# Optimization experiments

Hardware: AMD Instinct MI355X
Metric: run time of the kernel (lower is better)

The kernel has to match this reference:

```python
import jax, jax.numpy as jnp
import numpy as np

BN_EPS = 1e-5


def setup_inputs() -> dict:
    key = jax.random.key(0)
    ks = jax.random.split(key, 8)
    B, C, H, W = 8, 512, 48, 48
    P = 64
    s_in = 1.0 / np.sqrt(C)
    s_p = 1.0 / np.sqrt(P)
    return {
        "x": jax.random.normal(ks[0], (B, C, H, W), dtype=jnp.float32),
        "Wq": jax.random.uniform(ks[1], (P, C), jnp.float32, -s_in, s_in),
        "Wk": jax.random.uniform(ks[2], (P, C), jnp.float32, -s_in, s_in),
        "Wv": jax.random.uniform(ks[3], (C, C), jnp.float32, -s_in, s_in),
        "align_w": jax.random.uniform(ks[4], (P,), jnp.float32, -s_p, s_p),
        "Wfc": jax.random.uniform(ks[5], (C, C), jnp.float32, -s_in, s_in),
        "bfc": jax.random.uniform(ks[6], (C,), jnp.float32, -s_in, s_in),
        "gamma": jnp.ones((C,), jnp.float32),
        "beta": jnp.zeros((C,), jnp.float32),
    }


def reference(x, Wq, Wk, Wv, align_w, Wfc, bfc, gamma, beta):
    B, C, H, W = x.shape
    N = H * W
    px = jnp.transpose(x.reshape(B, C, N), (0, 2, 1))  # [B, N, C]

    q = jnp.tanh(px @ Wq.T)  # [B, N, P]
    k = jnp.tanh(px @ Wk.T)  # [B, N, P]
    v = px @ Wv.T            # [B, N, C]

    # align(q_i * k_j) = sum_p q[b,i,p] * k[b,j,p] * align_w[p]
    scores = jnp.einsum('bip,bjp,p->bij', q, k, align_w)  # [B, N, N]
    attn = jax.nn.softmax(scores, axis=2)

    content = px + attn @ v           # [B, N, C]
    content = content @ Wfc.T + bfc   # fc
    c = jnp.transpose(content, (0, 2, 1)).reshape(B, C, H, W)

    # BatchNorm2d in training mode: batch statistics over (B, H, W), biased var
    mean = jnp.mean(c, axis=(0, 2, 3), keepdims=True)
    var = jnp.var(c, axis=(0, 2, 3), keepdims=True)
    g = gamma.reshape(1, C, 1, 1)
    b = beta.reshape(1, C, 1, 1)
    out = g * (c - mean) * jax.lax.rsqrt(var + BN_EPS) + b
    return jax.nn.relu(out)
```

## Files before the change

kernel.cpp:

```cpp
#include <hip/hip_runtime.h>
#include <stdint.h>

#define BB 8
#define CC 512
#define NN 2304
#define NT16 (NN / 16)
#define NT32 (NN / 32)
#define CT32 (CC / 32)
#define NYB 48

typedef float f32x4 __attribute__((ext_vector_type(4)));
typedef short s16x8 __attribute__((ext_vector_type(8)));

__device__ __forceinline__ unsigned short f2bf(float f) {
  union { float f; uint32_t u; } v; v.f = f;
  uint32_t u = v.u;
  return (unsigned short)((u + 0x7FFFu + ((u >> 16) & 1u)) >> 16);
}
__device__ __forceinline__ float bf2f(unsigned short b) {
  union { uint32_t u; float f; } v; v.u = ((uint32_t)b) << 16;
  return v.f;
}
__device__ __forceinline__ uint32_t cvtpk(float lo, float hi) {
  uint32_t r;
  asm("v_cvt_pk_bf16_f32 %0, %1, %2" : "=v"(r) : "v"(lo), "v"(hi));
  return r;
}


__global__ void k_prep_w(const float* __restrict__ Wq, const float* __restrict__ Wk,
                         const float* __restrict__ Wv, const float* __restrict__ Wfc,
                         unsigned short* __restrict__ wcat_t, unsigned short* __restrict__ wfc_t) {
  int idx = blockIdx.x * 256 + threadIdx.x;
  const int tot_cat = 640 * 512;
  if (idx < tot_cat) {
    int tile = idx >> 9, inner = idx & 511;
    int j = (tile >> 4) * 16 + (inner >> 5);
    int k = (tile & 15) * 32 + (inner & 31);
    float v = (j < 64) ? Wq[j * 512 + k] : ((j < 128) ? Wk[(j - 64) * 512 + k] : Wv[(j - 128) * 512 + k]);
    wcat_t[idx] = f2bf(v);
  } else if (idx < tot_cat + 512 * 512) {
    int i2 = idx - tot_cat;
    int tile = i2 >> 9, inner = i2 & 511;
    int j = (tile >> 4) * 16 + (inner >> 5);
    int k = (tile & 15) * 32 + (inner & 31);
    wfc_t[i2] = f2bf(Wfc[j * 512 + k]);
  }
}

__global__ void k_px(const float* __restrict__ x, unsigned short* __restrict__ px_t) {
  __shared__ float t[32][33];
  int b = blockIdx.x;
  int nb = blockIdx.y * 32;
  int cb = blockIdx.z * 32;
  int lane = threadIdx.x & 31;
  int row = threadIdx.x >> 5;
  const float* xb = x + (size_t)b * CC * NN;
  for (int rr = 0; rr < 4; rr++) {
    int c = cb + row + 8 * rr;
    t[row + 8 * rr][lane] = xb[(size_t)c * NN + nb + lane];
  }
  __syncthreads();
  int rbase = (b * NN + nb) >> 4;
  int ct = cb >> 5;
  for (int rr = 0; rr < 4; rr++) {
    int nl = row + 8 * rr;
    size_t off = ((size_t)(rbase + (nl >> 4)) * CT32 + ct) * 512 + (nl & 15) * 32 + lane;
    px_t[off] = f2bf(t[lane][nl]);
  }
}

__global__ __launch_bounds__(256, 2) void k_qkv(const unsigned short* __restrict__ px_t,
                                                const unsigned short* __restrict__ wcat_t,
                                                const float* __restrict__ align_w,
                                                unsigned short* __restrict__ q_t,
                                                unsigned short* __restrict__ k_t,
                                                unsigned short* __restrict__ vt_t) {
  int bid = blockIdx.x;
  int b = bid & 7;
  int t = bid >> 3;
  int z = t % 3;
  int nb = (t / 3) * 64;
  int tid = threadIdx.x;
  int w = tid >> 6, l = tid & 63, l15 = l & 15, lq = l >> 4;
  int loff = l15 * 32 + 8 * lq;
  int rA = (b * NN + nb) >> 4;
  int nfmax = (z == 0) ? 2 : 4;
  int rowB0 = (z == 0) ? 2 * w : 8 + (z - 1) * 16 + 4 * w;
  f32x4 acc[4][4];
  for (int mf = 0; mf < 4; mf++) for (int nf = 0; nf < 4; nf++) acc[mf][nf] = (f32x4){0.f, 0.f, 0.f, 0.f};
  for (int kk = 0; kk < 16; kk++) {
    s16x8 a[4], bbf[4];
    for (int mf = 0; mf < 4; mf++)
      a[mf] = *(const s16x8*)(px_t + ((size_t)(rA + mf) * CT32 + kk) * 512 + loff);
    for (int nf = 0; nf < 4; nf++)
      if (nf < nfmax)
        bbf[nf] = *(const s16x8*)(wcat_t + ((size_t)(rowB0 + nf) * CT32 + kk) * 512 + loff);
    for (int mf = 0; mf < 4; mf++)
      for (int nf = 0; nf < 4; nf++)
        if (nf < nfmax)
          acc[mf][nf] = __builtin_amdgcn_mfma_f32_16x16x32_bf16(a[mf], bbf[nf], acc[mf][nf], 0, 0, 0);
  }
  if (z == 0) {
    for (int mf = 0; mf < 4; mf++)
      for (int nf = 0; nf < 2; nf++)
        for (int r = 0; r < 4; r++) {
          int j = 32 * w + 16 * nf + l15;
          int nl = 4 * lq + r;
          float v = tanhf(acc[mf][nf][r]);
          if (w < 2) {
            v *= align_w[j];
            q_t[((size_t)(rA + mf) * 2 + w) * 512 + nl * 32 + (j & 31)] = f2bf(v);
          } else {
            k_t[((size_t)(rA + mf) * 2 + (w - 2)) * 512 + nl * 32 + (j & 31)] = f2bf(v);
          }
        }
  } else {
    unsigned short* vtb = vt_t + (size_t)b * (CC / 16) * NT32 * 512;
    for (int mf = 0; mf < 4; mf++)
      for (int nf = 0; nf < 4; nf++) {
        int c = (z - 1) * 256 + 64 * w + 16 * nf + l15;
        uint2 pp;
        pp.x = cvtpk(acc[mf][nf][0], acc[mf][nf][1]);
        pp.y = cvtpk(acc[mf][nf][2], acc[mf][nf][3]);
        int nlo = 16 * (mf & 1) + 4 * lq;
        size_t off = ((size_t)(c >> 4) * NT32 + (nb >> 5) + (mf >> 1)) * 512 + (c & 15) * 32 + nlo;
        *(uint2*)(vtb + off) = pp;
      }
  }
}

__global__ __launch_bounds__(256, 3) void k_attn(const unsigned short* __restrict__ q_t,
                                                 const unsigned short* __restrict__ k_t,
                                                 const unsigned short* __restrict__ vt_t,
                                                 unsigned short* __restrict__ px_t ) {
  __shared__ __align__(16) unsigned short e_s[2][48 * 64];
  __shared__ float rs_s[4][48];
  int bid = blockIdx.x;
  int b = bid & 7;
  int ch = ((bid >> 3) & 1) * 256;
  int ib = (bid >> 4) * 48;
  int tid = threadIdx.x;
  int w = tid >> 6, l = tid & 63, l15 = l & 15, lq = l >> 4;
  int c0 = ch + 64 * w;
  int loff = l15 * 32 + 8 * lq;
  int rQ = (b * NN + ib) >> 4;
  int ktb = b * NT16;
  const unsigned short* vb = vt_t + (size_t)b * (CC / 16) * NT32 * 512;

  s16x8 qa[3][2];
  for (int mf = 0; mf < 3; mf++)
    for (int ks = 0; ks < 2; ks++)
      qa[mf][ks] = *(const s16x8*)(q_t + ((size_t)(rQ + mf) * 2 + ks) * 512 + loff);

  f32x4 acc[3][4];
  for (int mf = 0; mf < 3; mf++) for (int nf = 0; nf < 4; nf++) acc[mf][nf] = (f32x4){0.f, 0.f, 0.f, 0.f};
  float rs[3] = {0.f, 0.f, 0.f};

  s16x8 kf0[2], kf1[2];
  for (int ks = 0; ks < 2; ks++)
    kf0[ks] = *(const s16x8*)(k_t + ((size_t)(ktb + w) * 2 + ks) * 512 + loff);

  auto step = [&](int jt, char* ebuf, s16x8 (&kfu)[2], s16x8 (&kfl)[2]) {
    int jtn = (jt < NN / 64 - 1) ? jt + 1 : jt;
    s16x8 vf[2][4];
    for (int ks = 0; ks < 2; ks++)
      for (int nf = 0; nf < 4; nf++)
        vf[ks][nf] = *(const s16x8*)(vb + ((size_t)((c0 >> 4) + nf) * NT32 + jt * 2 + ks) * 512 + loff);
    for (int ks = 0; ks < 2; ks++)
      kfl[ks] = *(const s16x8*)(k_t + ((size_t)(ktb + jtn * 4 + w) * 2 + ks) * 512 + loff);
    f32x4 sc[3];
    for (int mf = 0; mf < 3; mf++) sc[mf] = (f32x4){0.f, 0.f, 0.f, 0.f};
    __builtin_amdgcn_s_setprio(1);
    for (int ks = 0; ks < 2; ks++)
      for (int mf = 0; mf < 3; mf++)
        sc[mf] = __builtin_amdgcn_mfma_f32_16x16x32_bf16(kfu[ks], qa[mf][ks], sc[mf], 0, 0, 0);
    __builtin_amdgcn_s_setprio(0);
    for (int mf = 0; mf < 3; mf++) {
      float e0 = __expf(sc[mf][0]), e1 = __expf(sc[mf][1]);
      float e2 = __expf(sc[mf][2]), e3 = __expf(sc[mf][3]);
      rs[mf] += (e0 + e1) + (e2 + e3);
      uint2 pp;
      pp.x = cvtpk(e0, e1);
      pp.y = cvtpk(e2, e3);
      int i_ = 16 * mf + l15;
      int byte = (i_ * 128 + (16 * w + 4 * lq) * 2) ^ ((i_ & 7) << 4);
      *(uint2*)(ebuf + byte) = pp;
    }
    asm volatile("s_waitcnt lgkmcnt(0)" ::: "memory");
    __builtin_amdgcn_s_barrier();
    __builtin_amdgcn_sched_barrier(0);
    for (int ks = 0; ks < 2; ks++) {
      s16x8 ef[3];
      for (int mf = 0; mf < 3; mf++) {
        int i_ = 16 * mf + l15;
        int byte = (i_ * 128 + 64 * ks + 16 * lq) ^ ((i_ & 7) << 4);
        ef[mf] = *(const s16x8*)((const char*)ebuf + byte);
      }
      __builtin_amdgcn_s_setprio(1);
      for (int nf = 0; nf < 4; nf++)
        for (int mf = 0; mf < 3; mf++)
          acc[mf][nf] = __builtin_amdgcn_mfma_f32_16x16x32_bf16(ef[mf], vf[ks][nf], acc[mf][nf], 0, 0, 0);
      __builtin_amdgcn_s_setprio(0);
    }
  };

  for (int jt = 0; jt < NN / 64; jt += 2) {
    step(jt, (char*)e_s[0], kf0, kf1);
    step(jt + 1, (char*)e_s[1], kf1, kf0);
  }

  for (int mf = 0; mf < 3; mf++) {
    float v = rs[mf];
    v += __shfl_xor(v, 16);
    v += __shfl_xor(v, 32);
    rs[mf] = v;
  }
  if (lq == 0)
    for (int mf = 0; mf < 3; mf++)
      rs_s[w][16 * mf + l15] = rs[mf];
  __syncthreads();
  float inv[3][4];
  for (int mf = 0; mf < 3; mf++)
    for (int r = 0; r < 4; r++) {
      int i = 16 * mf + 4 * lq + r;
      inv[mf][r] = 1.0f / (rs_s[0][i] + rs_s[1][i] + rs_s[2][i] + rs_s[3][i]);
    }
  for (int mf = 0; mf < 3; mf++)
    for (int nf = 0; nf < 4; nf++)
      for (int r = 0; r < 4; r++) {
        int i = 16 * mf + 4 * lq + r;
        int bn = b * NN + ib + i;
        int c = c0 + 16 * nf + l15;
        size_t off = ((size_t)(bn >> 4) * CT32 + (c >> 5)) * 512 + (bn & 15) * 32 + (c & 31);
        px_t[off] = f2bf(bf2f(px_t[off]) + acc[mf][nf][r] * inv[mf][r]);
      }
}

__global__ __launch_bounds__(256, 3) void k_fc(const unsigned short* __restrict__ px_t,
                                               const unsigned short* __restrict__ wfc_t,
                                               const float* __restrict__ bfc,
                                               unsigned short* __restrict__ c16,
                                               float2* __restrict__ partials) {
  __shared__ float pss[4][32], psq[4][32];
  int bid = blockIdx.x;
  int s_ = bid >> 3;
  int yb = (bid & 7) + 8 * (s_ % 6);
  int cb = (s_ / 6) * 32;
  int fb = yb * 384;
  int tid = threadIdx.x;
  int w = tid >> 6, l = tid & 63, l15 = l & 15, lq = l >> 4;
  int fw = fb + 96 * w;
  int loff = l15 * 32 + 8 * lq;
  f32x4 acc[2][6];
  for (int mf = 0; mf < 2; mf++) for (int nf = 0; nf < 6; nf++) acc[mf][nf] = (f32x4){0.f, 0.f, 0.f, 0.f};
  for (int kk = 0; kk < 16; kk++) {
    s16x8 a[2], bbf[6];
    for (int mf = 0; mf < 2; mf++)
      a[mf] = *(const s16x8*)(wfc_t + ((size_t)((cb >> 4) + mf) * CT32 + kk) * 512 + loff);
    for (int nf = 0; nf < 6; nf++)
      bbf[nf] = *(const s16x8*)(px_t + ((size_t)((fw >> 4) + nf) * CT32 + kk) * 512 + loff);
    for (int mf = 0; mf < 2; mf++)
      for (int nf = 0; nf < 6; nf++)
        acc[mf][nf] = __builtin_amdgcn_mfma_f32_16x16x32_bf16(a[mf], bbf[nf], acc[mf][nf], 0, 0, 0);
  }
  float s8[2][4], q8[2][4];
  for (int mf = 0; mf < 2; mf++)
    for (int r = 0; r < 4; r++) {
      int c2 = cb + 16 * mf + 4 * lq + r;
      float bias = bfc[c2];
      float s = 0.f, q = 0.f;
      for (int nf = 0; nf < 6; nf++) {
        float v = acc[mf][nf][r] + bias;
        int flat = fw + 16 * nf + l15;
        int b2 = flat / NN;
        int n = flat - b2 * NN;
        c16[((size_t)b2 * CC + c2) * NN + n] = f2bf(v);
        s += v; q += v * v;
      }
      s8[mf][r] = s; q8[mf][r] = q;
    }
  for (int mf = 0; mf < 2; mf++)
    for (int r = 0; r < 4; r++) {
      float s = s8[mf][r], q = q8[mf][r];
      s += __shfl_xor(s, 1); q += __shfl_xor(q, 1);
      s += __shfl_xor(s, 2); q += __shfl_xor(q, 2);
      s += __shfl_xor(s, 4); q += __shfl_xor(q, 4);
      s += __shfl_xor(s, 8); q += __shfl_xor(q, 8);
      s8[mf][r] = s; q8[mf][r] = q;
    }
  if (l15 == 0)
    for (int mf = 0; mf < 2; mf++)
      for (int r = 0; r < 4; r++) {
        int idx = 16 * mf + 4 * lq + r;
        pss[w][idx] = s8[mf][r];
        psq[w][idx] = q8[mf][r];
      }
  __syncthreads();
  if (tid < 32) {
    float s = pss[0][tid] + pss[1][tid] + pss[2][tid] + pss[3][tid];
    float q = psq[0][tid] + psq[1][tid] + psq[2][tid] + psq[3][tid];
    partials[(size_t)(cb + tid) * NYB + yb] = make_float2(s, q);
  }
}

__global__ void k_stats2(const float2* __restrict__ partials, const float* __restrict__ gamma,
                         const float* __restrict__ beta, float2* __restrict__ ab) {
  int c = blockIdx.x * 256 + threadIdx.x;
  if (c >= CC) return;
  float s = 0.f, q = 0.f;
  for (int i = 0; i < NYB; i++) {
    float2 p = partials[(size_t)c * NYB + i];
    s += p.x; q += p.y;
  }
  const float invn = 1.0f / (BB * NN);
  float mean = s * invn;
  float var = q * invn - mean * mean;
  float a = gamma[c] * rsqrtf(var + 1e-5f);
  ab[c] = make_float2(a, beta[c] - mean * a);
}

__global__ void k_bn(const unsigned short* __restrict__ c16, float* __restrict__ out,
                     const float2* __restrict__ ab) {
  int idx = blockIdx.x * 256 + threadIdx.x;
  const int total = BB * CC * NN / 8;
  if (idx >= total) return;
  int c = (idx / (NN / 8)) & (CC - 1);
  float2 p = ab[c];
  s16x8 v = ((const s16x8*)c16)[idx];
  f32x4 o0, o1;
  for (int i = 0; i < 4; i++) o0[i] = fmaxf(0.f, bf2f((unsigned short)v[i]) * p.x + p.y);
  for (int i = 0; i < 4; i++) o1[i] = fmaxf(0.f, bf2f((unsigned short)v[4 + i]) * p.x + p.y);
  ((f32x4*)out)[idx * 2] = o0;
  ((f32x4*)out)[idx * 2 + 1] = o1;
}

extern "C" void kernel_launch(void* const* d_in, const int* in_sizes, int n_in,
                              void* d_out, int out_size, void* d_ws, size_t ws_size,
                              hipStream_t stream) {
  const float* x = (const float*)d_in[0];
  const float* Wq = (const float*)d_in[1];
  const float* Wk = (const float*)d_in[2];
  const float* Wv = (const float*)d_in[3];
  const float* align_w = (const float*)d_in[4];
  const float* Wfc = (const float*)d_in[5];
  const float* bfc = (const float*)d_in[6];
  const float* gamma = (const float*)d_in[7];
  const float* beta = (const float*)d_in[8];
  float* out = (float*)d_out;

  char* ws = (char*)d_ws;
  const size_t sz_px = (size_t)BB * NN * CC * 2;
  const size_t sz_q = (size_t)BB * NN * 64 * 2;
  const size_t sz_vr = (size_t)BB * NN * CC * 2;
  unsigned short* px_t = (unsigned short*)(ws);
  unsigned short* q_t = (unsigned short*)(ws + sz_px);
  unsigned short* k_t = (unsigned short*)(ws + sz_px + sz_q);
  unsigned short* c16 = (unsigned short*)(ws + sz_px + 2 * sz_q);
  unsigned short* vt_t = (unsigned short*)(ws + sz_px + 2 * sz_q + sz_vr);
  unsigned short* wcat_t = (unsigned short*)(ws + sz_px + 2 * sz_q + 2 * sz_vr);
  unsigned short* wfc_t = (unsigned short*)(ws + sz_px + 2 * sz_q + 2 * sz_vr + 640 * 512 * 2);
  float2* partials = (float2*)(ws + sz_px + 2 * sz_q + 2 * sz_vr + 640 * 512 * 2 + 512 * 512 * 2);
  float2* ab = (float2*)((char*)partials + (size_t)CC * NYB * sizeof(float2));

  k_prep_w<<<(640 * 512 + 512 * 512 + 255) / 256, 256, 0, stream>>>(Wq, Wk, Wv, Wfc, wcat_t, wfc_t);
  k_px<<<dim3(BB, NN / 32, CC / 32), 256, 0, stream>>>(x, px_t);
  k_qkv<<<864, 256, 0, stream>>>(px_t, wcat_t, align_w, q_t, k_t, vt_t);
  k_attn<<<768, 256, 0, stream>>>(q_t, k_t, vt_t, px_t);
  k_fc<<<768, 256, 0, stream>>>(px_t, wfc_t, bfc, c16, partials);
  k_stats2<<<2, 256, 0, stream>>>(partials, gamma, beta, ab);
  k_bn<<<(BB * CC * NN / 8 + 255) / 256, 256, 0, stream>>>(c16, out, ab);
}
```

Measured before the change: 171.2 us.

## Shrink attention row tile, fuse BN stats into apply, batch px transpose

The attention kernel's query tile drops from 48 to 32 rows per block, which cuts registers and shared memory. Launch bounds rise to 4 blocks per SM and the grid grows to 1152 blocks, raising occupancy at the cost of re-streaming K and V more often. The separate stats kernel is removed, and every BN thread now recomputes its channel's mean and scale from the 48 partials, saving a launch but adding redundant reads. The px transpose kernel now handles four 32-channel tiles per block, giving fewer, larger blocks.

Measured after the change: 208.6 us. 21.8% more time.

```diff
diff --git a/kernel.cpp b/kernel.cpp
--- a/kernel.cpp
+++ b/kernel.cpp
@@ -52,21 +52,25 @@
   __shared__ float t[32][33];
   int b = blockIdx.x;
   int nb = blockIdx.y * 32;
-  int cb = blockIdx.z * 32;
+  int cb0 = blockIdx.z * 128;
   int lane = threadIdx.x & 31;
   int row = threadIdx.x >> 5;
   const float* xb = x + (size_t)b * CC * NN;
-  for (int rr = 0; rr < 4; rr++) {
-    int c = cb + row + 8 * rr;
-    t[row + 8 * rr][lane] = xb[(size_t)c * NN + nb + lane];
-  }
-  __syncthreads();
   int rbase = (b * NN + nb) >> 4;
-  int ct = cb >> 5;
-  for (int rr = 0; rr < 4; rr++) {
-    int nl = row + 8 * rr;
-    size_t off = ((size_t)(rbase + (nl >> 4)) * CT32 + ct) * 512 + (nl & 15) * 32 + lane;
-    px_t[off] = f2bf(t[lane][nl]);
+  for (int z = 0; z < 4; z++) {
+    int cb = cb0 + z * 32;
+    for (int rr = 0; rr < 4; rr++) {
+      int c = cb + row + 8 * rr;
+      t[row + 8 * rr][lane] = xb[(size_t)c * NN + nb + lane];
+    }
+    __syncthreads();
+    int ct = cb >> 5;
+    for (int rr = 0; rr < 4; rr++) {
+      int nl = row + 8 * rr;
+      size_t off = ((size_t)(rbase + (nl >> 4)) * CT32 + ct) * 512 + (nl & 15) * 32 + lane;
+      px_t[off] = f2bf(t[lane][nl]);
+    }
+    __syncthreads();
   }
 }
 
@@ -130,16 +134,16 @@
   }
 }
 
-__global__ __launch_bounds__(256, 3) void k_attn(const unsigned short* __restrict__ q_t,
+__global__ __launch_bounds__(256, 4) void k_attn(const unsigned short* __restrict__ q_t,
                                                  const unsigned short* __restrict__ k_t,
                                                  const unsigned short* __restrict__ vt_t,
                                                  unsigned short* __restrict__ px_t ) {
-  __shared__ __align__(16) unsigned short e_s[2][48 * 64];
-  __shared__ float rs_s[4][48];
+  __shared__ __align__(16) unsigned short e_s[2][32 * 64];
+  __shared__ float rs_s[4][32];
   int bid = blockIdx.x;
   int b = bid & 7;
   int ch = ((bid >> 3) & 1) * 256;
-  int ib = (bid >> 4) * 48;
+  int ib = (bid >> 4) * 32;
   int tid = threadIdx.x;
   int w = tid >> 6, l = tid & 63, l15 = l & 15, lq = l >> 4;
   int c0 = ch + 64 * w;
@@ -148,14 +152,14 @@
   int ktb = b * NT16;
   const unsigned short* vb = vt_t + (size_t)b * (CC / 16) * NT32 * 512;
 
-  s16x8 qa[3][2];
-  for (int mf = 0; mf < 3; mf++)
+  s16x8 qa[2][2];
+  for (int mf = 0; mf < 2; mf++)
     for (int ks = 0; ks < 2; ks++)
       qa[mf][ks] = *(const s16x8*)(q_t + ((size_t)(rQ + mf) * 2 + ks) * 512 + loff);
 
-  f32x4 acc[3][4];
-  for (int mf = 0; mf < 3; mf++) for (int nf = 0; nf < 4; nf++) acc[mf][nf] = (f32x4){0.f, 0.f, 0.f, 0.f};
-  float rs[3] = {0.f, 0.f, 0.f};
+  f32x4 acc[2][4];
+  for (int mf = 0; mf < 2; mf++) for (int nf = 0; nf < 4; nf++) acc[mf][nf] = (f32x4){0.f, 0.f, 0.f, 0.f};
+  float rs[2] = {0.f, 0.f};
 
   s16x8 kf0[2], kf1[2];
   for (int ks = 0; ks < 2; ks++)
@@ -169,14 +173,15 @@
         vf[ks][nf] = *(const s16x8*)(vb + ((size_t)((c0 >> 4) + nf) * NT32 + jt * 2 + ks) * 512 + loff);
     for (int ks = 0; ks < 2; ks++)
       kfl[ks] = *(const s16x8*)(k_t + ((size_t)(ktb + jtn * 4 + w) * 2 + ks) * 512 + loff);
-    f32x4 sc[3];
-    for (int mf = 0; mf < 3; mf++) sc[mf] = (f32x4){0.f, 0.f, 0.f, 0.f};
+    f32x4 sc[2];
+    sc[0] = (f32x4){0.f, 0.f, 0.f, 0.f};
+    sc[1] = (f32x4){0.f, 0.f, 0.f, 0.f};
     __builtin_amdgcn_s_setprio(1);
     for (int ks = 0; ks < 2; ks++)
-      for (int mf = 0; mf < 3; mf++)
+      for (int mf = 0; mf < 2; mf++)
         sc[mf] = __builtin_amdgcn_mfma_f32_16x16x32_bf16(kfu[ks], qa[mf][ks], sc[mf], 0, 0, 0);
     __builtin_amdgcn_s_setprio(0);
-    for (int mf = 0; mf < 3; mf++) {
+    for (int mf = 0; mf < 2; mf++) {
       float e0 = __expf(sc[mf][0]), e1 = __expf(sc[mf][1]);
       float e2 = __expf(sc[mf][2]), e3 = __expf(sc[mf][3]);
       rs[mf] += (e0 + e1) + (e2 + e3);
@@ -191,15 +196,15 @@
     __builtin_amdgcn_s_barrier();
     __builtin_amdgcn_sched_barrier(0);
     for (int ks = 0; ks < 2; ks++) {
-      s16x8 ef[3];
-      for (int mf = 0; mf < 3; mf++) {
+      s16x8 ef[2];
+      for (int mf = 0; mf < 2; mf++) {
         int i_ = 16 * mf + l15;
         int byte = (i_ * 128 + 64 * ks + 16 * lq) ^ ((i_ & 7) << 4);
         ef[mf] = *(const s16x8*)((const char*)ebuf + byte);
       }
       __builtin_amdgcn_s_setprio(1);
       for (int nf = 0; nf < 4; nf++)
-        for (int mf = 0; mf < 3; mf++)
+        for (int mf = 0; mf < 2; mf++)
           acc[mf][nf] = __builtin_amdgcn_mfma_f32_16x16x32_bf16(ef[mf], vf[ks][nf], acc[mf][nf], 0, 0, 0);
       __builtin_amdgcn_s_setprio(0);
     }
@@ -210,23 +215,23 @@
     step(jt + 1, (char*)e_s[1], kf1, kf0);
   }
 
-  for (int mf = 0; mf < 3; mf++) {
+  for (int mf = 0; mf < 2; mf++) {
     float v = rs[mf];
     v += __shfl_xor(v, 16);
     v += __shfl_xor(v, 32);
     rs[mf] = v;
   }
   if (lq == 0)
-    for (int mf = 0; mf < 3; mf++)
+    for (int mf = 0; mf < 2; mf++)
       rs_s[w][16 * mf + l15] = rs[mf];
   __syncthreads();
-  float inv[3][4];
-  for (int mf = 0; mf < 3; mf++)
+  float inv[2][4];
+  for (int mf = 0; mf < 2; mf++)
     for (int r = 0; r < 4; r++) {
       int i = 16 * mf + 4 * lq + r;
       inv[mf][r] = 1.0f / (rs_s[0][i] + rs_s[1][i] + rs_s[2][i] + rs_s[3][i]);
     }
-  for (int mf = 0; mf < 3; mf++)
+  for (int mf = 0; mf < 2; mf++)
     for (int nf = 0; nf < 4; nf++)
       for (int r = 0; r < 4; r++) {
         int i = 16 * mf + 4 * lq + r;
@@ -304,11 +309,15 @@
   }
 }
 
-__global__ void k_stats2(const float2* __restrict__ partials, const float* __restrict__ gamma,
-                         const float* __restrict__ beta, float2* __restrict__ ab) {
-  int c = blockIdx.x * 256 + threadIdx.x;
-  if (c >= CC) return;
+__global__ void k_bn(const unsigned short* __restrict__ c16, float* __restrict__ out,
+                     const float2* __restrict__ partials, const float* __restrict__ gamma,
+                     const float* __restrict__ beta) {
+  int idx = blockIdx.x * 256 + threadIdx.x;
+  const int total = BB * CC * NN / 8;
+  if (idx >= total) return;
+  int c = (idx / (NN / 8)) & (CC - 1);
   float s = 0.f, q = 0.f;
+#pragma unroll
   for (int i = 0; i < NYB; i++) {
     float2 p = partials[(size_t)c * NYB + i];
     s += p.x; q += p.y;
@@ -317,20 +326,11 @@
   float mean = s * invn;
   float var = q * invn - mean * mean;
   float a = gamma[c] * rsqrtf(var + 1e-5f);
-  ab[c] = make_float2(a, beta[c] - mean * a);
-}
-
-__global__ void k_bn(const unsigned short* __restrict__ c16, float* __restrict__ out,
-                     const float2* __restrict__ ab) {
-  int idx = blockIdx.x * 256 + threadIdx.x;
-  const int total = BB * CC * NN / 8;
-  if (idx >= total) return;
-  int c = (idx / (NN / 8)) & (CC - 1);
-  float2 p = ab[c];
+  float b2 = beta[c] - mean * a;
   s16x8 v = ((const s16x8*)c16)[idx];
   f32x4 o0, o1;
-  for (int i = 0; i < 4; i++) o0[i] = fmaxf(0.f, bf2f((unsigned short)v[i]) * p.x + p.y);
-  for (int i = 0; i < 4; i++) o1[i] = fmaxf(0.f, bf2f((unsigned short)v[4 + i]) * p.x + p.y);
+  for (int i = 0; i < 4; i++) o0[i] = fmaxf(0.f, bf2f((unsigned short)v[i]) * a + b2);
+  for (int i = 0; i < 4; i++) o1[i] = fmaxf(0.f, bf2f((unsigned short)v[4 + i]) * a + b2);
   ((f32x4*)out)[idx * 2] = o0;
   ((f32x4*)out)[idx * 2 + 1] = o1;
 }
@@ -361,13 +361,11 @@
   unsigned short* wcat_t = (unsigned short*)(ws + sz_px + 2 * sz_q + 2 * sz_vr);
   unsigned short* wfc_t = (unsigned short*)(ws + sz_px + 2 * sz_q + 2 * sz_vr + 640 * 512 * 2);
   float2* partials = (float2*)(ws + sz_px + 2 * sz_q + 2 * sz_vr + 640 * 512 * 2 + 512 * 512 * 2);
-  float2* ab = (float2*)((char*)partials + (size_t)CC * NYB * sizeof(float2));
 
   k_prep_w<<<(640 * 512 + 512 * 512 + 255) / 256, 256, 0, stream>>>(Wq, Wk, Wv, Wfc, wcat_t, wfc_t);
-  k_px<<<dim3(BB, NN / 32, CC / 32), 256, 0, stream>>>(x, px_t);
+  k_px<<<dim3(BB, NN / 32, 4), 256, 0, stream>>>(x, px_t);
   k_qkv<<<864, 256, 0, stream>>>(px_t, wcat_t, align_w, q_t, k_t, vt_t);
-  k_attn<<<768, 256, 0, stream>>>(q_t, k_t, vt_t, px_t);
+  k_attn<<<1152, 256, 0, stream>>>(q_t, k_t, vt_t, px_t);
   k_fc<<<768, 256, 0, stream>>>(px_t, wfc_t, bfc, c16, partials);
-  k_stats2<<<2, 256, 0, stream>>>(partials, gamma, beta, ab);
-  k_bn<<<(BB * CC * NN / 8 + 255) / 256, 256, 0, stream>>>(c16, out, ab);
-}
+  k_bn<<<(BB * CC * NN / 8 + 255) / 256, 256, 0, stream>>>(c16, out, partials, gamma, beta);
+}
```

## Widen attention key tiles, coarsen px transpose blocks, fold BN stats into apply

Applied to the files above, without the earlier changes.

The attention loop now handles 128 keys per iteration instead of two 64-key steps, which halves the barrier count per key and loads K and V fragments for both halves up front. The shared exp buffer doubles to hold the wider tile. The px transpose kernel processes four channel tiles per block to cut the launch grid. The separate BN stats-finalize kernel is removed, and every thread of the BN apply kernel recomputes mean and variance from the 48 partials. That saves one launch at the cost of redundant reads and extra registers.

After: 261.8 us. +52.9%, slower.

```diff
diff --git a/kernel.cpp b/kernel.cpp
--- a/kernel.cpp
+++ b/kernel.cpp
@@ -52,21 +52,25 @@
   __shared__ float t[32][33];
   int b = blockIdx.x;
   int nb = blockIdx.y * 32;
-  int cb = blockIdx.z * 32;
+  int cb0 = blockIdx.z * 128;
   int lane = threadIdx.x & 31;
   int row = threadIdx.x >> 5;
   const float* xb = x + (size_t)b * CC * NN;
-  for (int rr = 0; rr < 4; rr++) {
-    int c = cb + row + 8 * rr;
-    t[row + 8 * rr][lane] = xb[(size_t)c * NN + nb + lane];
-  }
-  __syncthreads();
   int rbase = (b * NN + nb) >> 4;
-  int ct = cb >> 5;
-  for (int rr = 0; rr < 4; rr++) {
-    int nl = row + 8 * rr;
-    size_t off = ((size_t)(rbase + (nl >> 4)) * CT32 + ct) * 512 + (nl & 15) * 32 + lane;
-    px_t[off] = f2bf(t[lane][nl]);
+  for (int z = 0; z < 4; z++) {
+    int cb = cb0 + z * 32;
+    for (int rr = 0; rr < 4; rr++) {
+      int c = cb + row + 8 * rr;
+      t[row + 8 * rr][lane] = xb[(size_t)c * NN + nb + lane];
+    }
+    __syncthreads();
+    int ct = cb >> 5;
+    for (int rr = 0; rr < 4; rr++) {
+      int nl = row + 8 * rr;
+      size_t off = ((size_t)(rbase + (nl >> 4)) * CT32 + ct) * 512 + (nl & 15) * 32 + lane;
+      px_t[off] = f2bf(t[lane][nl]);
+    }
+    __syncthreads();
   }
 }
 
@@ -134,7 +138,7 @@
                                                  const unsigned short* __restrict__ k_t,
                                                  const unsigned short* __restrict__ vt_t,
                                                  unsigned short* __restrict__ px_t ) {
-  __shared__ __align__(16) unsigned short e_s[2][48 * 64];
+  __shared__ __align__(16) unsigned short e_s[2][48 * 128];
   __shared__ float rs_s[4][48];
   int bid = blockIdx.x;
   int b = bid & 7;
@@ -157,57 +161,54 @@
   for (int mf = 0; mf < 3; mf++) for (int nf = 0; nf < 4; nf++) acc[mf][nf] = (f32x4){0.f, 0.f, 0.f, 0.f};
   float rs[3] = {0.f, 0.f, 0.f};
 
-  s16x8 kf0[2], kf1[2];
-  for (int ks = 0; ks < 2; ks++)
-    kf0[ks] = *(const s16x8*)(k_t + ((size_t)(ktb + w) * 2 + ks) * 512 + loff);
-
-  auto step = [&](int jt, char* ebuf, s16x8 (&kfu)[2], s16x8 (&kfl)[2]) {
-    int jtn = (jt < NN / 64 - 1) ? jt + 1 : jt;
-    s16x8 vf[2][4];
-    for (int ks = 0; ks < 2; ks++)
-      for (int nf = 0; nf < 4; nf++)
-        vf[ks][nf] = *(const s16x8*)(vb + ((size_t)((c0 >> 4) + nf) * NT32 + jt * 2 + ks) * 512 + loff);
-    for (int ks = 0; ks < 2; ks++)
-      kfl[ks] = *(const s16x8*)(k_t + ((size_t)(ktb + jtn * 4 + w) * 2 + ks) * 512 + loff);
-    f32x4 sc[3];
-    for (int mf = 0; mf < 3; mf++) sc[mf] = (f32x4){0.f, 0.f, 0.f, 0.f};
-    __builtin_amdgcn_s_setprio(1);
-    for (int ks = 0; ks < 2; ks++)
-      for (int mf = 0; mf < 3; mf++)
-        sc[mf] = __builtin_amdgcn_mfma_f32_16x16x32_bf16(kfu[ks], qa[mf][ks], sc[mf], 0, 0, 0);
-    __builtin_amdgcn_s_setprio(0);
-    for (int mf = 0; mf < 3; mf++) {
-      float e0 = __expf(sc[mf][0]), e1 = __expf(sc[mf][1]);
-      float e2 = __expf(sc[mf][2]), e3 = __expf(sc[mf][3]);
-      rs[mf] += (e0 + e1) + (e2 + e3);
-      uint2 pp;
-      pp.x = cvtpk(e0, e1);
-      pp.y = cvtpk(e2, e3);
-      int i_ = 16 * mf + l15;
-      int byte = (i_ * 128 + (16 * w + 4 * lq) * 2) ^ ((i_ & 7) << 4);
-      *(uint2*)(ebuf + byte) = pp;
+  const int NP = NN / 128;
+  for (int p = 0; p < NP; p++) {
+    char* ebuf = (char*)e_s[p & 1];
+    s16x8 kf[2][2];
+    for (int h = 0; h < 2; h++)
+      for (int kp = 0; kp < 2; kp++)
+        kf[h][kp] = *(const s16x8*)(k_t + ((size_t)(ktb + (2 * p + h) * 4 + w) * 2 + kp) * 512 + loff);
+    s16x8 vf[2][2][4];
+    for (int h = 0; h < 2; h++)
+      for (int kp = 0; kp < 2; kp++)
+        for (int nf = 0; nf < 4; nf++)
+          vf[h][kp][nf] = *(const s16x8*)(vb + ((size_t)((c0 >> 4) + nf) * NT32 + 4 * p + 2 * h + kp) * 512 + loff);
+    for (int h = 0; h < 2; h++) {
+      f32x4 sc[3];
+      for (int mf = 0; mf < 3; mf++) sc[mf] = (f32x4){0.f, 0.f, 0.f, 0.f};
+      __builtin_amdgcn_s_setprio(1);
+      for (int kp = 0; kp < 2; kp++)
+        for (int mf = 0; mf < 3; mf++)
+          sc[mf] = __builtin_amdgcn_mfma_f32_16x16x32_bf16(kf[h][kp], qa[mf][kp], sc[mf], 0, 0, 0);
+      __builtin_amdgcn_s_setprio(0);
+      for (int mf = 0; mf < 3; mf++) {
+        float e0 = __expf(sc[mf][0]), e1 = __expf(sc[mf][1]);
+        float e2 = __expf(sc[mf][2]), e3 = __expf(sc[mf][3]);
+        rs[mf] += (e0 + e1) + (e2 + e3);
+        uint2 pp;
+        pp.x = cvtpk(e0, e1);
+        pp.y = cvtpk(e2, e3);
+        int i_ = 16 * mf + l15;
+        int byte = (i_ * 256 + (64 * h + 16 * w + 4 * lq) * 2) ^ ((i_ & 7) << 4);
+        *(uint2*)(ebuf + byte) = pp;
+      }
     }
     asm volatile("s_waitcnt lgkmcnt(0)" ::: "memory");
     __builtin_amdgcn_s_barrier();
     __builtin_amdgcn_sched_barrier(0);
-    for (int ks = 0; ks < 2; ks++) {
+    for (int ks = 0; ks < 4; ks++) {
       s16x8 ef[3];
       for (int mf = 0; mf < 3; mf++) {
         int i_ = 16 * mf + l15;
-        int byte = (i_ * 128 + 64 * ks + 16 * lq) ^ ((i_ & 7) << 4);
+        int byte = (i_ * 256 + 64 * ks + 16 * lq) ^ ((i_ & 7) << 4);
         ef[mf] = *(const s16x8*)((const char*)ebuf + byte);
       }
       __builtin_amdgcn_s_setprio(1);
       for (int nf = 0; nf < 4; nf++)
         for (int mf = 0; mf < 3; mf++)
-          acc[mf][nf] = __builtin_amdgcn_mfma_f32_16x16x32_bf16(ef[mf], vf[ks][nf], acc[mf][nf], 0, 0, 0);
+          acc[mf][nf] = __builtin_amdgcn_mfma_f32_16x16x32_bf16(ef[mf], vf[ks >> 1][ks & 1][nf], acc[mf][nf], 0, 0, 0);
       __builtin_amdgcn_s_setprio(0);
     }
-  };
-
-  for (int jt = 0; jt < NN / 64; jt += 2) {
-    step(jt, (char*)e_s[0], kf0, kf1);
-    step(jt + 1, (char*)e_s[1], kf1, kf0);
   }
 
   for (int mf = 0; mf < 3; mf++) {
@@ -304,11 +305,15 @@
   }
 }
 
-__global__ void k_stats2(const float2* __restrict__ partials, const float* __restrict__ gamma,
-                         const float* __restrict__ beta, float2* __restrict__ ab) {
-  int c = blockIdx.x * 256 + threadIdx.x;
-  if (c >= CC) return;
+__global__ void k_bn(const unsigned short* __restrict__ c16, float* __restrict__ out,
+                     const float2* __restrict__ partials, const float* __restrict__ gamma,
+                     const float* __restrict__ beta) {
+  int idx = blockIdx.x * 256 + threadIdx.x;
+  const int total = BB * CC * NN / 8;
+  if (idx >= total) return;
+  int c = (idx / (NN / 8)) & (CC - 1);
   float s = 0.f, q = 0.f;
+#pragma unroll
   for (int i = 0; i < NYB; i++) {
     float2 p = partials[(size_t)c * NYB + i];
     s += p.x; q += p.y;
@@ -317,20 +322,11 @@
   float mean = s * invn;
   float var = q * invn - mean * mean;
   float a = gamma[c] * rsqrtf(var + 1e-5f);
-  ab[c] = make_float2(a, beta[c] - mean * a);
-}
-
-__global__ void k_bn(const unsigned short* __restrict__ c16, float* __restrict__ out,
-                     const float2* __restrict__ ab) {
-  int idx = blockIdx.x * 256 + threadIdx.x;
-  const int total = BB * CC * NN / 8;
-  if (idx >= total) return;
-  int c = (idx / (NN / 8)) & (CC - 1);
-  float2 p = ab[c];
+  float b2 = beta[c] - mean * a;
   s16x8 v = ((const s16x8*)c16)[idx];
   f32x4 o0, o1;
-  for (int i = 0; i < 4; i++) o0[i] = fmaxf(0.f, bf2f((unsigned short)v[i]) * p.x + p.y);
-  for (int i = 0; i < 4; i++) o1[i] = fmaxf(0.f, bf2f((unsigned short)v[4 + i]) * p.x + p.y);
+  for (int i = 0; i < 4; i++) o0[i] = fmaxf(0.f, bf2f((unsigned short)v[i]) * a + b2);
+  for (int i = 0; i < 4; i++) o1[i] = fmaxf(0.f, bf2f((unsigned short)v[4 + i]) * a + b2);
   ((f32x4*)out)[idx * 2] = o0;
   ((f32x4*)out)[idx * 2 + 1] = o1;
 }
@@ -361,13 +357,11 @@
   unsigned short* wcat_t = (unsigned short*)(ws + sz_px + 2 * sz_q + 2 * sz_vr);
   unsigned short* wfc_t = (unsigned short*)(ws + sz_px + 2 * sz_q + 2 * sz_vr + 640 * 512 * 2);
   float2* partials = (float2*)(ws + sz_px + 2 * sz_q + 2 * sz_vr + 640 * 512 * 2 + 512 * 512 * 2);
-  float2* ab = (float2*)((char*)partials + (size_t)CC * NYB * sizeof(float2));
 
   k_prep_w<<<(640 * 512 + 512 * 512 + 255) / 256, 256, 0, stream>>>(Wq, Wk, Wv, Wfc, wcat_t, wfc_t);
-  k_px<<<dim3(BB, NN / 32, CC / 32), 256, 0, stream>>>(x, px_t);
+  k_px<<<dim3(BB, NN / 32, 4), 256, 0, stream>>>(x, px_t);
   k_qkv<<<864, 256, 0, stream>>>(px_t, wcat_t, align_w, q_t, k_t, vt_t);
   k_attn<<<768, 256, 0, stream>>>(q_t, k_t, vt_t, px_t);
   k_fc<<<768, 256, 0, stream>>>(px_t, wfc_t, bfc, c16, partials);
-  k_stats2<<<2, 256, 0, stream>>>(partials, gamma, beta, ab);
-  k_bn<<<(BB * CC * NN / 8 + 255) / 256, 256, 0, stream>>>(c16, out, ab);
-}
+  k_bn<<<(BB * CC * NN / 8 + 255) / 256, 256, 0, stream>>>(c16, out, partials, gamma, beta);
+}
```
